# Optimization experiments

Measured on AMD Instinct MI355X. Metric: run time of the kernel, lower is better.

## Reference

```python
import jax, jax.numpy as jnp
import numpy as np

HEADS, HID, OUT_C, IN_C = 8, 128, 2, 64
D = HID // HEADS
NODE = {"cell0": 50000, "cell1": 100000, "cell2": 25000}
# (src_type, dst_type, edge_name, num_edges)
ETYPES = [("cell0", "cell0", "u00", 200000),
          ("cell1", "cell1", "u11", 200000),
          ("cell1", "cell0", "b10", 100000),
          ("cell2", "cell1", "b21", 50000)]


def _segment_softmax(scores, seg, num_segments):
    # numerically-stable softmax over irregular destination segments
    m = jax.ops.segment_max(scores, seg, num_segments=num_segments)
    e = jnp.exp(scores - m[seg])
    s = jax.ops.segment_sum(e, seg, num_segments=num_segments)
    return e / (s[seg] + 1e-16)


def setup_inputs() -> dict:
    key = jax.random.key(0)
    ks = iter(jax.random.split(key, 64))
    s = 0.1
    inp = {}
    for nt, n in NODE.items():
        inp[f"x_{nt}"] = jax.random.normal(next(ks), (n, IN_C), jnp.float32)
    for st, dt, name, e in ETYPES:
        src = jax.random.randint(next(ks), (e,), 0, NODE[st], jnp.int32)
        dst = jax.random.randint(next(ks), (e,), 0, NODE[dt], jnp.int32)
        inp[f"ei_{name}"] = jnp.stack([src, dst])
    # HANConv params: per node-type projection, per edge-type attention vectors
    for nt in NODE:
        inp[f"W_{nt}"] = jax.random.normal(next(ks), (IN_C, HID), jnp.float32) * s
        inp[f"b_{nt}"] = jnp.zeros((HID,), jnp.float32)
    for _, _, name, _ in ETYPES:
        inp[f"as_{name}"] = jax.random.normal(next(ks), (HEADS, D), jnp.float32) * s
        inp[f"ad_{name}"] = jax.random.normal(next(ks), (HEADS, D), jnp.float32) * s
    # semantic attention params + final classifier
    inp["k_w"] = jax.random.normal(next(ks), (HID, HID), jnp.float32) * s
    inp["k_b"] = jnp.zeros((HID,), jnp.float32)
    inp["q"] = jax.random.normal(next(ks), (HID,), jnp.float32) * s
    inp["lin_w"] = jax.random.normal(next(ks), (HID, OUT_C), jnp.float32) * s
    inp["lin_b"] = jnp.zeros((OUT_C,), jnp.float32)
    return inp


def _han_conv(x, ei, W, b, att_s, att_d, k_w, k_b, q):
    # node-level: project each node type -> [N, H, D]
    h = {nt: (x[nt] @ W[nt] + b[nt]).reshape(-1, HEADS, D) for nt in NODE}
    outs = {nt: [] for nt in NODE}
    for st, dt, name, _ in ETYPES:
        xs, xd = h[st], h[dt]
        a_s = (xs * att_s[name]).sum(-1)  # [Ns, H]
        a_d = (xd * att_d[name]).sum(-1)  # [Nd, H]
        src, dst = ei[name][0], ei[name][1]
        alpha = jax.nn.leaky_relu(a_s[src] + a_d[dst], 0.2)  # [E, H]
        alpha = _segment_softmax(alpha, dst, NODE[dt])
        msg = xs[src] * alpha[:, :, None]  # [E, H, D]
        agg = jax.ops.segment_sum(msg, dst, num_segments=NODE[dt])
        outs[dt].append(jax.nn.relu(agg.reshape(-1, HID)))
    # semantic-level attention across metapaths per dst node type
    res = {}
    for nt, lst in outs.items():
        if not lst:
            res[nt] = None
            continue
        stk = jnp.stack(lst)  # [M, N, HID]
        score = (q * jnp.tanh(stk @ k_w + k_b).mean(1)).sum(-1)  # [M]
        attn = jax.nn.softmax(score)
        res[nt] = jnp.einsum('m,mnf->nf', attn, stk)
    return res


def reference(x_cell0, x_cell1, x_cell2,
              W_cell0, b_cell0, W_cell1, b_cell1, W_cell2, b_cell2,
              as_u00, ad_u00, as_u11, ad_u11, as_b10, ad_b10, as_b21, ad_b21,
              k_w, k_b, q, lin_w, lin_b,
              ei_u00, ei_u11, ei_b10, ei_b21):
    x = {"cell0": x_cell0, "cell1": x_cell1, "cell2": x_cell2}
    ei = {"u00": ei_u00, "u11": ei_u11, "b10": ei_b10, "b21": ei_b21}
    W = {"cell0": W_cell0, "cell1": W_cell1, "cell2": W_cell2}
    b = {"cell0": b_cell0, "cell1": b_cell1, "cell2": b_cell2}
    att_s = {"u00": as_u00, "u11": as_u11, "b10": as_b10, "b21": as_b21}
    att_d = {"u00": ad_u00, "u11": ad_u11, "b10": ad_b10, "b21": ad_b21}
    # HAN.forward calls han_conv twice with identical inputs (first result
    # discarded); in eval mode (dropout off) both calls are identical math,
    # so we compute it once.
    out = _han_conv(x, ei, W, b, att_s, att_d, k_w, k_b, q)
    pooled = sum(jnp.sum(v, axis=0) for v in out.values() if v is not None)  # global_add_pool, batch=None
    return jax.nn.sigmoid(pooled[None, :] @ lin_w + lin_b)  # [1, OUT_C]
```

## Files before the change

kernel.cpp:

```cpp
#include <hip/hip_runtime.h>
#include <hip/hip_fp16.h>

#define N0 50000
#define N1 100000
#define N2 25000
#define E00 200000
#define E11 200000
#define E10 100000
#define E21 50000
#define EE  550000
#define ND  300000
#define NB  293
#define NT_ALL 18750
#define HID 128
#define INC 64

typedef _Float16 half8 __attribute__((ext_vector_type(8)));
typedef _Float16 half4_t __attribute__((ext_vector_type(4)));
typedef float float4v __attribute__((ext_vector_type(4)));
typedef float floatx2 __attribute__((ext_vector_type(2)));

struct PrepT {
    const float* W; const float* bias;
    const float* av0; const float* av1; const float* av2; const float* av3;
    _Float16* wtg; _Float16* adtg; float* bdc;
};

__device__ __forceinline__ void decode_edge(
    int e, const int* ei00, const int* ei10, const int* ei11, const int* ei21,
    int& src, int& slot)
{
    if (e < E00)                    { src = ei00[e];               slot = ei00[E00 + e]; }
    else if (e < E00 + E10)         { int i = e - E00;             src = ei10[i]; slot = 50000  + ei10[E10 + i]; }
    else if (e < E00 + E10 + E11)   { int i = e - E00 - E10;       src = ei11[i]; slot = 100000 + ei11[E11 + i]; }
    else                            { int i = e - E00 - E10 - E11; src = ei21[i]; slot = 200000 + ei21[E21 + i]; }
}

__global__ __launch_bounds__(256) void prep_kernel(
    PrepT p0, PrepT p1, PrepT p2,
    const float* __restrict__ kw, const float* __restrict__ lw,
    unsigned char* __restrict__ kwf8,
    const int* __restrict__ ei00, const int* __restrict__ ei10,
    const int* __restrict__ ei11, const int* __restrict__ ei21,
    int* __restrict__ cnt)
{
    if (blockIdx.x >= 32) {
        int e = (blockIdx.x - 32) * 256 + threadIdx.x;
        if (e >= EE) return;
        int src, slot;
        decode_edge(e, ei00, ei10, ei11, ei21, src, slot);
        atomicAdd(&cnt[slot], 1);
        return;
    }
    if (blockIdx.x >= 24) {
        int base = (blockIdx.x - 24) * 256 + threadIdx.x;
        for (int it = 0; it < 9; ++it) {
            int idx = base + it * 2048;
            int f = idx >> 7, g = idx & 127;
            float v;
            if (f < 128)      v = kw[g * 128 + f];
            else if (f < 130) v = lw[g * 2 + (f - 128)];
            else              v = 0.f;
            int r = __builtin_amdgcn_cvt_pk_fp8_f32(v, 0.f, 0, false);
            kwf8[idx] = (unsigned char)r;
        }
        return;
    }
    PrepT P = (blockIdx.x >= 16) ? p2 : (blockIdx.x >= 8) ? p1 : p0;
    const int lb = blockIdx.x & 7;
    const int t2 = lb * 256 + threadIdx.x;
    {
        int f = t2 >> 4, g0 = (t2 & 15) * 4;
        half4_t v;
#pragma unroll
        for (int j = 0; j < 4; ++j) v[j] = (_Float16)P.W[(g0 + j) * 128 + f];
        *(half4_t*)&P.wtg[f * 64 + g0] = v;
    }
    {
        int c = t2 >> 6, g = t2 & 63;
        const float* av = (c < 8) ? P.av0 : (c < 16) ? P.av1 : (c < 24) ? P.av2 : P.av3;
        float v = 0.f;
        if (av) {
            int hh = c & 7;
#pragma unroll
            for (int d = 0; d < 16; ++d)
                v += P.W[g * 128 + hh * 16 + d] * av[hh * 16 + d];
        }
        P.adtg[c * 64 + g] = (_Float16)v;
    }
    if (lb == 0 && threadIdx.x < 32) {
        int c = threadIdx.x;
        const float* av = (c < 8) ? P.av0 : (c < 16) ? P.av1 : (c < 24) ? P.av2 : P.av3;
        float v = 0.f;
        if (av) {
            int hh = c & 7;
#pragma unroll
            for (int d = 0; d < 16; ++d)
                v += P.bias[hh * 16 + d] * av[hh * 16 + d];
        }
        P.bdc[c] = v;
    }
}

struct PT {
    const float* x; const float* bias; unsigned char* h;
    float* ao0; float* ao1; float* ao2; float* ao3;
    const _Float16* wtg; const _Float16* adtg; const float* bdc;
    int N; int ntiles; int bstart; int nblocks;
};

#define HPAD 136
#define PROJ_BLKS 1024

__global__ __launch_bounds__(256, 2) void proj_mfma(
    PT t0, PT t1, PT t2,
    const int* __restrict__ cnt, int* __restrict__ part)
{
    __shared__ _Float16 ht[4][16][HPAD];
    __shared__ int swt[4];
    const int tid = threadIdx.x;
    const int lane = tid & 63, wv = tid >> 6;
    const int fi = lane & 15, hi = lane >> 4;

    if (blockIdx.x >= PROJ_BLKS) {
        const int b = blockIdx.x - PROJ_BLKS;
        int i0 = b * 1024 + tid * 4;
        int s = 0;
#pragma unroll
        for (int k = 0; k < 4; ++k) { int i = i0 + k; s += (i < ND) ? cnt[i] : 0; }
#pragma unroll
        for (int off = 1; off < 64; off <<= 1) s += __shfl_xor(s, off);
        if ((tid & 63) == 0) swt[tid >> 6] = s;
        __syncthreads();
        if (tid == 0) part[b] = swt[0] + swt[1] + swt[2] + swt[3];
        return;
    }

    PT A = (blockIdx.x >= t2.bstart) ? t2 : (blockIdx.x >= t1.bstart) ? t1 : t0;

    half8 bfr[8][2], bd[2][2];
#pragma unroll
    for (int nt = 0; nt < 8; ++nt)
#pragma unroll
        for (int kb = 0; kb < 2; ++kb)
            bfr[nt][kb] = *(const half8*)&A.wtg[(nt * 16 + fi) * 64 + kb * 32 + hi * 8];
#pragma unroll
    for (int t = 0; t < 2; ++t)
#pragma unroll
        for (int kb = 0; kb < 2; ++kb)
            bd[t][kb] = *(const half8*)&A.adtg[(t * 16 + fi) * 64 + kb * 32 + hi * 8];

    float bvv[8];
#pragma unroll
    for (int nt = 0; nt < 8; ++nt) bvv[nt] = A.bias[nt * 16 + fi];
    const float bdc0 = A.bdc[fi];
    const float bdc1 = A.bdc[16 + fi];

    float* aolo = (fi >= 8) ? A.ao1 : A.ao0;
    float* aohi = (fi >= 8) ? A.ao3 : A.ao2;
    const bool has_hi = (A.ao2 != nullptr) || (A.ao3 != nullptr);

    const int stride = A.nblocks * 4;
    for (int t = (blockIdx.x - A.bstart) * 4 + wv; t < A.ntiles; t += stride) {
        const int base = t * 16;
        int rsrc = base + fi; if (rsrc >= A.N) rsrc = A.N - 1;
        const float* xp = A.x + (size_t)rsrc * 64 + hi * 8;
        float4 u0 = *(const float4*)(xp);
        float4 u1 = *(const float4*)(xp + 4);
        float4 u2 = *(const float4*)(xp + 32);
        float4 u3 = *(const float4*)(xp + 36);
        half8 a0, a1;
        a0[0] = (_Float16)u0.x; a0[1] = (_Float16)u0.y; a0[2] = (_Float16)u0.z; a0[3] = (_Float16)u0.w;
        a0[4] = (_Float16)u1.x; a0[5] = (_Float16)u1.y; a0[6] = (_Float16)u1.z; a0[7] = (_Float16)u1.w;
        a1[0] = (_Float16)u2.x; a1[1] = (_Float16)u2.y; a1[2] = (_Float16)u2.z; a1[3] = (_Float16)u2.w;
        a1[4] = (_Float16)u3.x; a1[5] = (_Float16)u3.y; a1[6] = (_Float16)u3.z; a1[7] = (_Float16)u3.w;

        float4v c[8];
#pragma unroll
        for (int nt = 0; nt < 8; ++nt) {
            float4v z = {0.f, 0.f, 0.f, 0.f};
            z = __builtin_amdgcn_mfma_f32_16x16x32_f16(a0, bfr[nt][0], z, 0, 0, 0);
            z = __builtin_amdgcn_mfma_f32_16x16x32_f16(a1, bfr[nt][1], z, 0, 0, 0);
            c[nt] = z;
        }
        float4v d0 = {0.f, 0.f, 0.f, 0.f};
        d0 = __builtin_amdgcn_mfma_f32_16x16x32_f16(a0, bd[0][0], d0, 0, 0, 0);
        d0 = __builtin_amdgcn_mfma_f32_16x16x32_f16(a1, bd[0][1], d0, 0, 0, 0);
        float4v d1 = {0.f, 0.f, 0.f, 0.f};
        if (has_hi) {
            d1 = __builtin_amdgcn_mfma_f32_16x16x32_f16(a0, bd[1][0], d1, 0, 0, 0);
            d1 = __builtin_amdgcn_mfma_f32_16x16x32_f16(a1, bd[1][1], d1, 0, 0, 0);
        }

#pragma unroll
        for (int nt = 0; nt < 8; ++nt)
#pragma unroll
            for (int r = 0; r < 4; ++r)
                ht[wv][hi * 4 + r][nt * 16 + fi] = (_Float16)(c[nt][r] + bvv[nt]);
#pragma unroll
        for (int i = 0; i < 4; ++i) {
            int row = i * 4 + hi;
            int node = base + row;
            if (node < A.N) {
                half8 v = *(const half8*)&ht[wv][row][fi * 8];
                int pa = __builtin_amdgcn_cvt_pk_fp8_f32((float)v[0], (float)v[1], 0, false);
                pa = __builtin_amdgcn_cvt_pk_fp8_f32((float)v[2], (float)v[3], pa, true);
                int pb = __builtin_amdgcn_cvt_pk_fp8_f32((float)v[4], (float)v[5], 0, false);
                pb = __builtin_amdgcn_cvt_pk_fp8_f32((float)v[6], (float)v[7], pb, true);
                int2 o = {pa, pb};
                *(int2*)(A.h + (size_t)node * 128 + fi * 8) = o;
            }
        }
        if (aolo) {
#pragma unroll
            for (int r = 0; r < 4; ++r) {
                int node = base + hi * 4 + r;
                if (node < A.N) aolo[(size_t)node * 8 + (fi & 7)] = d0[r] + bdc0;
            }
        }
        if (aohi) {
#pragma unroll
            for (int r = 0; r < 4; ++r) {
                int node = base + hi * 4 + r;
                if (node < A.N) aohi[(size_t)node * 8 + (fi & 7)] = d1[r] + bdc1;
            }
        }
    }
}

__global__ __launch_bounds__(256) void scan23_kernel(
    const int* __restrict__ cnt, const int* __restrict__ part,
    int* __restrict__ off, int* __restrict__ cursor)
{
    __shared__ int sd[256];
    __shared__ int pex[512];
    __shared__ int wt[4];
    const int tid = threadIdx.x, b = blockIdx.x;
    const int lane = tid & 63, wv = tid >> 6;

    int p0 = (2 * tid     < NB) ? part[2 * tid]     : 0;
    int p1 = (2 * tid + 1 < NB) ? part[2 * tid + 1] : 0;
    int ps = p0 + p1;
    sd[tid] = ps; __syncthreads();
    for (int d = 1; d < 256; d <<= 1) {
        int v = (tid >= d) ? sd[tid - d] : 0;
        __syncthreads();
        sd[tid] += v;
        __syncthreads();
    }
    int exc = sd[tid] - ps;
    pex[2 * tid] = exc;
    pex[2 * tid + 1] = exc + p0;
    __syncthreads();

    int i0 = b * 1024 + tid * 4;
    int v[4];
#pragma unroll
    for (int k = 0; k < 4; ++k) { int i = i0 + k; v[k] = (i < ND) ? cnt[i] : 0; }
    int ts = v[0] + v[1] + v[2] + v[3];
    int inc = ts;
#pragma unroll
    for (int d = 1; d < 64; d <<= 1) {
        int u = __shfl_up(inc, d);
        if (lane >= d) inc += u;
    }
    int wexc = inc - ts;
    if (lane == 63) wt[wv] = inc;
    __syncthreads();
    int wbase = 0;
    for (int w = 0; w < wv; ++w) wbase += wt[w];
    int base = pex[b] + wbase + wexc;
    int pre = 0;
#pragma unroll
    for (int k = 0; k < 4; ++k) {
        int i = i0 + k;
        if (i < ND) { off[i] = base + pre; cursor[i] = base + pre; }
        pre += v[k];
    }
}

__global__ __launch_bounds__(256) void fill_kernel(
    const int* __restrict__ ei00, const int* __restrict__ ei10,
    const int* __restrict__ ei11, const int* __restrict__ ei21,
    const float* __restrict__ as00, const float* __restrict__ ad00,
    const float* __restrict__ as10, const float* __restrict__ ad10,
    const float* __restrict__ as11, const float* __restrict__ ad11,
    const float* __restrict__ as21, const float* __restrict__ ad21,
    int* __restrict__ cursor, int* __restrict__ srcs, _Float16* __restrict__ wgt)
{
    int e = blockIdx.x * 256 + threadIdx.x;
    if (e >= EE) return;
    int src, d, slot;
    const float* asp; const float* adp;
    if (e < E00) {
        src = ei00[e]; d = ei00[E00 + e]; slot = d; asp = as00; adp = ad00;
    } else if (e < E00 + E10) {
        int i = e - E00; src = ei10[i]; d = ei10[E10 + i]; slot = 50000 + d; asp = as10; adp = ad10;
    } else if (e < E00 + E10 + E11) {
        int i = e - E00 - E10; src = ei11[i]; d = ei11[E11 + i]; slot = 100000 + d; asp = as11; adp = ad11;
    } else {
        int i = e - E00 - E10 - E11; src = ei21[i]; d = ei21[E21 + i]; slot = 200000 + d; asp = as21; adp = ad21;
    }
    float4 sa0 = *(const float4*)(asp + (size_t)src * 8);
    float4 sa1 = *(const float4*)(asp + (size_t)src * 8 + 4);
    float4 da0 = *(const float4*)(adp + (size_t)d * 8);
    float4 da1 = *(const float4*)(adp + (size_t)d * 8 + 4);
    float vv[8] = {sa0.x + da0.x, sa0.y + da0.y, sa0.z + da0.z, sa0.w + da0.w,
                   sa1.x + da1.x, sa1.y + da1.y, sa1.z + da1.z, sa1.w + da1.w};
    half8 w;
#pragma unroll
    for (int h = 0; h < 8; ++h) {
        float v = vv[h];
        v = v > 0.f ? v : 0.2f * v;
        w[h] = (_Float16)__expf(v);
    }
    int pos = atomicAdd(&cursor[slot], 1);
    srcs[pos] = src;
    *(half8*)(wgt + (size_t)pos * 8) = w;
}

__global__ __launch_bounds__(256) void gather_kernel(
    const int* __restrict__ cnt, const int* __restrict__ off,
    const int* __restrict__ srcs, const _Float16* __restrict__ wgt,
    const unsigned char* __restrict__ h0, const unsigned char* __restrict__ h1,
    const unsigned char* __restrict__ h2,
    unsigned char* __restrict__ agg)
{
    const int gid = blockIdx.x * 256 + threadIdx.x;
    const int lane = gid & 63;
    const int g8 = lane >> 3, sub = lane & 7;
    const int slot = (gid >> 6) * 8 + g8;
    const unsigned char* hs = (slot < 50000) ? h0 : (slot < 200000) ? h1 : h2;
    const int deg = cnt[slot], st = off[slot];

    int degm = deg;
    degm = max(degm, __shfl_xor(degm, 8));
    degm = max(degm, __shfl_xor(degm, 16));
    degm = max(degm, __shfl_xor(degm, 32));

    float acc[16];
#pragma unroll
    for (int j = 0; j < 16; ++j) acc[j] = 0.f;
    float sw = 0.f;

    int i = 0;
    for (; i + 2 <= degm; i += 2) {
        bool a0 = (i < deg), a1 = (i + 1 < deg);
        int s0 = 0, s1 = 0;
        if (a0) s0 = srcs[st + i];
        if (a1) s1 = srcs[st + i + 1];
        float w0 = 0.f, w1 = 0.f;
        int4 v0 = {0, 0, 0, 0}, v1 = {0, 0, 0, 0};
        if (a0) { w0 = (float)wgt[(size_t)(st + i) * 8 + sub];
                  v0 = *(const int4*)(hs + (size_t)s0 * 128 + sub * 16); }
        if (a1) { w1 = (float)wgt[(size_t)(st + i + 1) * 8 + sub];
                  v1 = *(const int4*)(hs + (size_t)s1 * 128 + sub * 16); }
        const int wa[4] = {v0.x, v0.y, v0.z, v0.w};
        const int wb[4] = {v1.x, v1.y, v1.z, v1.w};
#pragma unroll
        for (int k = 0; k < 4; ++k) {
            floatx2 fa0 = __builtin_amdgcn_cvt_pk_f32_fp8(wa[k], false);
            floatx2 fa1 = __builtin_amdgcn_cvt_pk_f32_fp8(wa[k], true);
            floatx2 fb0 = __builtin_amdgcn_cvt_pk_f32_fp8(wb[k], false);
            floatx2 fb1 = __builtin_amdgcn_cvt_pk_f32_fp8(wb[k], true);
            acc[4 * k + 0] += w0 * fa0.x + w1 * fb0.x;
            acc[4 * k + 1] += w0 * fa0.y + w1 * fb0.y;
            acc[4 * k + 2] += w0 * fa1.x + w1 * fb1.x;
            acc[4 * k + 3] += w0 * fa1.y + w1 * fb1.y;
        }
        sw += w0 + w1;
    }
    if (i < degm) {
        bool a0 = (i < deg);
        int s0 = 0;
        if (a0) s0 = srcs[st + i];
        float w0 = 0.f;
        int4 v0 = {0, 0, 0, 0};
        if (a0) { w0 = (float)wgt[(size_t)(st + i) * 8 + sub];
                  v0 = *(const int4*)(hs + (size_t)s0 * 128 + sub * 16); }
        const int wa[4] = {v0.x, v0.y, v0.z, v0.w};
#pragma unroll
        for (int k = 0; k < 4; ++k) {
            floatx2 fa0 = __builtin_amdgcn_cvt_pk_f32_fp8(wa[k], false);
            floatx2 fa1 = __builtin_amdgcn_cvt_pk_f32_fp8(wa[k], true);
            acc[4 * k + 0] += w0 * fa0.x;
            acc[4 * k + 1] += w0 * fa0.y;
            acc[4 * k + 2] += w0 * fa1.x;
            acc[4 * k + 3] += w0 * fa1.y;
        }
        sw += w0;
    }

    float rr = __builtin_amdgcn_rcpf(sw + 1e-16f);
    int4 o;
    int pk[4];
#pragma unroll
    for (int k = 0; k < 4; ++k) {
        float r0 = fmaxf(acc[4 * k + 0] * rr, 0.f);
        float r1 = fmaxf(acc[4 * k + 1] * rr, 0.f);
        float r2 = fmaxf(acc[4 * k + 2] * rr, 0.f);
        float r3 = fmaxf(acc[4 * k + 3] * rr, 0.f);
        int p = __builtin_amdgcn_cvt_pk_fp8_f32(r0, r1, 0, false);
        p = __builtin_amdgcn_cvt_pk_fp8_f32(r2, r3, p, true);
        pk[k] = p;
    }
    o.x = pk[0]; o.y = pk[1]; o.z = pk[2]; o.w = pk[3];
    *(int4*)(agg + (size_t)slot * 128 + sub * 16) = o;
}

#define ASTR 144
__global__ __launch_bounds__(256, 2) void semantic_kernel(
    const unsigned char* __restrict__ agg, const unsigned char* __restrict__ kwf8,
    const float* __restrict__ kb, const float* __restrict__ q,
    const float* __restrict__ lb,
    float* __restrict__ cs2, float* __restrict__ score,
    unsigned int* __restrict__ done, float* __restrict__ out)
{
    __shared__ char abuf[2][16 * ASTR];
    __shared__ float redv[12];
    const int tid = threadIdx.x;
    const int lane = tid & 63, wv = tid >> 6;
    const int fi = lane & 15, hi = lane >> 4;

    if (tid < 12) redv[tid] = 0.f;

    const int ftbase = wv * 2;
    const int nft = (wv == 3) ? 3 : 2;

    long bf[3][4];
    float qv[3], kbv[3];
#pragma unroll
    for (int i = 0; i < 3; ++i) {
        if (i < nft) {
            int ft = ftbase + i;
#pragma unroll
            for (int kk = 0; kk < 4; ++kk)
                bf[i][kk] = *(const long*)&kwf8[(ft * 16 + fi) * 128 + kk * 32 + hi * 8];
            qv[i]  = (ft < 8) ? q[ft * 16 + fi]  : 0.f;
            kbv[i] = (ft < 8) ? kb[ft * 16 + fi] : 0.f;
        } else {
            bf[i][0] = bf[i][1] = bf[i][2] = bf[i][3] = 0;
            qv[i] = 0.f; kbv[i] = 0.f;
        }
    }

    float sc[4] = {0.f, 0.f, 0.f, 0.f};
    float cs[4] = {0.f, 0.f, 0.f, 0.f};

    const int s_off = (tid >> 4) * ASTR + (tid & 15) * 8;
    const int a_off = fi * ASTR + hi * 8;

    int t = blockIdx.x;
    const int stride = gridDim.x;
    if (t < NT_ALL) {
        long areg = *(const long*)(agg + (size_t)t * 2048 + tid * 8);
        *(long*)&abuf[0][s_off] = areg;
    }
    __syncthreads();
    int cur = 0;
    while (t < NT_ALL) {
        const int tn = t + stride;
        long aregn = 0;
        if (tn < NT_ALL)
            aregn = *(const long*)(agg + (size_t)tn * 2048 + tid * 8);

        long af[4];
#pragma unroll
        for (int kk = 0; kk < 4; ++kk)
            af[kk] = *(const long*)&abuf[cur][a_off + kk * 32];

        const int m = (t >= 12500) ? 3 : (t >= 6250) ? 2 : (t >= 3125) ? 1 : 0;
        float tsc = 0.f, tcs = 0.f;
#pragma unroll
        for (int i = 0; i < 3; ++i) {
            if (i >= nft) continue;
            float4v c = {0.f, 0.f, 0.f, 0.f};
            c = __builtin_amdgcn_mfma_f32_16x16x32_fp8_fp8(af[0], bf[i][0], c, 0, 0, 0);
            c = __builtin_amdgcn_mfma_f32_16x16x32_fp8_fp8(af[1], bf[i][1], c, 0, 0, 0);
            c = __builtin_amdgcn_mfma_f32_16x16x32_fp8_fp8(af[2], bf[i][2], c, 0, 0, 0);
            c = __builtin_amdgcn_mfma_f32_16x16x32_fp8_fp8(af[3], bf[i][3], c, 0, 0, 0);
            if (ftbase + i == 8) {
                tcs = c[0] + c[1] + c[2] + c[3];
            } else {
#pragma unroll
                for (int r = 0; r < 4; ++r) {
                    float y = c[r] + kbv[i];
                    float e = __expf(2.f * y);
                    tsc += qv[i] * (1.f - 2.f * __builtin_amdgcn_rcpf(e + 1.f));
                }
            }
        }
        if (m == 0)      { sc[0] += tsc; cs[0] += tcs; }
        else if (m == 1) { sc[1] += tsc; cs[1] += tcs; }
        else if (m == 2) { sc[2] += tsc; cs[2] += tcs; }
        else             { sc[3] += tsc; cs[3] += tcs; }

        if (tn < NT_ALL)
            *(long*)&abuf[cur ^ 1][s_off] = aregn;
        __syncthreads();
        cur ^= 1;
        t = tn;
    }

#pragma unroll
    for (int m = 0; m < 4; ++m) {
        float s = sc[m];
#pragma unroll
        for (int off = 1; off < 64; off <<= 1) s += __shfl_xor(s, off);
        if (lane == 0 && s != 0.f) atomicAdd(&redv[m], s);
        float v = cs[m];
        v += __shfl_xor(v, 16);
        v += __shfl_xor(v, 32);
        if (hi == 0 && fi < 2 && v != 0.f) atomicAdd(&redv[4 + 2 * m + fi], v);
    }
    __syncthreads();
    if (tid < 4)              atomicAdd(&score[tid], redv[tid]);
    if (tid >= 4 && tid < 12) atomicAdd(&cs2[tid - 4], redv[tid]);

    __syncthreads();
    if (tid == 0) {
        __threadfence();
        unsigned int old = atomicAdd(done, 1u);
        if (old == gridDim.x - 1) {
            __threadfence();
            float s0 = score[0] / (float)N0;
            float s1 = score[1] / (float)N0;
            float s2 = score[2] / (float)N1;
            float s3 = score[3] / (float)N1;
            float m0 = fmaxf(s0, s1);
            float e0 = __expf(s0 - m0), e1 = __expf(s1 - m0);
            float a0 = e0 / (e0 + e1), a1 = e1 / (e0 + e1);
            float m1 = fmaxf(s2, s3);
            float e2 = __expf(s2 - m1), e3 = __expf(s3 - m1);
            float a2 = e2 / (e2 + e3), a3 = e3 / (e2 + e3);
            float z0 = a0 * cs2[0] + a1 * cs2[2] + a2 * cs2[4] + a3 * cs2[6] + lb[0];
            float z1 = a0 * cs2[1] + a1 * cs2[3] + a2 * cs2[5] + a3 * cs2[7] + lb[1];
            out[0] = 1.f / (1.f + __expf(-z0));
            out[1] = 1.f / (1.f + __expf(-z1));
        }
    }
}

extern "C" void kernel_launch(void* const* d_in, const int* in_sizes, int n_in,
                              void* d_out, int out_size, void* d_ws, size_t ws_size,
                              hipStream_t stream)
{
    const float* x0  = (const float*)d_in[0];
    const float* x1  = (const float*)d_in[1];
    const float* x2  = (const float*)d_in[2];
    const int* ei00  = (const int*)d_in[3];
    const int* ei11  = (const int*)d_in[4];
    const int* ei10  = (const int*)d_in[5];
    const int* ei21  = (const int*)d_in[6];
    const float* W0  = (const float*)d_in[7];  const float* b0 = (const float*)d_in[8];
    const float* W1  = (const float*)d_in[9];  const float* b1 = (const float*)d_in[10];
    const float* W2  = (const float*)d_in[11]; const float* b2 = (const float*)d_in[12];
    const float* as00 = (const float*)d_in[13]; const float* ad00 = (const float*)d_in[14];
    const float* as11 = (const float*)d_in[15]; const float* ad11 = (const float*)d_in[16];
    const float* as10 = (const float*)d_in[17]; const float* ad10 = (const float*)d_in[18];
    const float* as21 = (const float*)d_in[19]; const float* ad21 = (const float*)d_in[20];
    const float* kw  = (const float*)d_in[21]; const float* kb  = (const float*)d_in[22];
    const float* q   = (const float*)d_in[23];
    const float* lw  = (const float*)d_in[24]; const float* lb  = (const float*)d_in[25];
    float* out = (float*)d_out;

    char* p = (char*)d_ws;
    auto alloc = [&](size_t bytes) {
        char* r = p;
        p += (bytes + 255) & ~(size_t)255;
        return r;
    };
    unsigned char* h0 = (unsigned char*)alloc((size_t)N0 * 128);
    unsigned char* h1 = (unsigned char*)alloc((size_t)N1 * 128);
    unsigned char* h2 = (unsigned char*)alloc((size_t)N2 * 128);
    float* o_as00 = (float*)alloc((size_t)N0 * 32);
    float* o_ad00 = (float*)alloc((size_t)N0 * 32);
    float* o_as11 = (float*)alloc((size_t)N1 * 32);
    float* o_ad11 = (float*)alloc((size_t)N1 * 32);
    float* o_as10 = (float*)alloc((size_t)N1 * 32);
    float* o_ad10 = (float*)alloc((size_t)N0 * 32);
    float* o_as21 = (float*)alloc((size_t)N2 * 32);
    float* o_ad21 = (float*)alloc((size_t)N1 * 32);
    int* off    = (int*)alloc((size_t)ND * 4);
    int* cursor = (int*)alloc((size_t)ND * 4);
    int* part   = (int*)alloc((size_t)512 * 4);
    int* srcs   = (int*)alloc((size_t)EE * 4);
    _Float16* wgt = (_Float16*)alloc((size_t)EE * 16);
    unsigned char* agg = (unsigned char*)alloc((size_t)ND * 128);
    _Float16* wtg0 = (_Float16*)alloc(128 * 64 * 2);
    _Float16* wtg1 = (_Float16*)alloc(128 * 64 * 2);
    _Float16* wtg2 = (_Float16*)alloc(128 * 64 * 2);
    _Float16* adtg0 = (_Float16*)alloc(32 * 64 * 2);
    _Float16* adtg1 = (_Float16*)alloc(32 * 64 * 2);
    _Float16* adtg2 = (_Float16*)alloc(32 * 64 * 2);
    float* bdcg = (float*)alloc(3 * 32 * 4);
    unsigned char* kwf8 = (unsigned char*)alloc(144 * 128);
    char* zstart = p;
    int* cnt = (int*)alloc((size_t)ND * 4);
    float* colsum2 = (float*)alloc(8 * 4);
    float* score   = (float*)alloc(4 * 4);
    unsigned int* done = (unsigned int*)alloc(4);
    size_t zbytes = (size_t)(p - zstart);

    (void)hipMemsetAsync(zstart, 0, zbytes, stream);

    PrepT pp0 = {W0, b0, as00, ad00, ad10, nullptr, wtg0, adtg0, bdcg + 0};
    PrepT pp1 = {W1, b1, as11, ad11, as10, ad21,    wtg1, adtg1, bdcg + 32};
    PrepT pp2 = {W2, b2, as21, nullptr, nullptr, nullptr, wtg2, adtg2, bdcg + 64};
    prep_kernel<<<32 + (EE + 255) / 256, 256, 0, stream>>>(
        pp0, pp1, pp2, kw, lw, kwf8, ei00, ei10, ei11, ei21, cnt);

    PT t0 = {x0, b0, h0,
             o_as00, o_ad00, o_ad10, nullptr,
             wtg0, adtg0, bdcg + 0,
             N0, 3125, 0, 296};
    PT t1 = {x1, b1, h1,
             o_as11, o_ad11, o_as10, o_ad21,
             wtg1, adtg1, bdcg + 32,
             N1, 6250, 296, 584};
    PT t2 = {x2, b2, h2,
             o_as21, nullptr, nullptr, nullptr,
             wtg2, adtg2, bdcg + 64,
             N2, 1563, 880, 144};
    proj_mfma<<<PROJ_BLKS + NB, 256, 0, stream>>>(t0, t1, t2, cnt, part);

    scan23_kernel<<<NB, 256, 0, stream>>>(cnt, part, off, cursor);

    fill_kernel<<<(EE + 255) / 256, 256, 0, stream>>>(ei00, ei10, ei11, ei21,
        o_as00, o_ad00, o_as10, o_ad10, o_as11, o_ad11, o_as21, o_ad21,
        cursor, srcs, wgt);

    gather_kernel<<<ND / 32, 256, 0, stream>>>(cnt, off, srcs, wgt, h0, h1, h2, agg);

    semantic_kernel<<<2048, 256, 0, stream>>>(agg, kwf8, kb, q, lb,
                                              colsum2, score, done, out);
}
```

Measured before the change: 301.9 us.

## Fuse gather aggregation with semantic attention scoring via shared-memory tile

Merges the gather kernel and the semantic kernel into one launch. Each block aggregates 32 destination slots, writes the fp8 results into an LDS tile, and runs the semantic MFMA scoring on that tile in place. This removes the global round-trip of the aggregated buffer and one kernel launch. In exchange every one of the 9375 blocks reloads the kw weights from global or cache, pays extra block-level and global atomic reductions, and increments the done counter, where the old semantic kernel used 2048 persistent blocks.

New measurement: 458.8 us. 52.0% more time.

```diff
diff --git a/kernel.cpp b/kernel.cpp
--- a/kernel.cpp
+++ b/kernel.cpp
@@ -11,7 +11,6 @@
 #define EE  550000
 #define ND  300000
 #define NB  293
-#define NT_ALL 18750
 #define HID 128
 #define INC 64
 
@@ -319,17 +318,27 @@
     *(half8*)(wgt + (size_t)pos * 8) = w;
 }
 
-__global__ __launch_bounds__(256) void gather_kernel(
+#define ATSTR 136
+__global__ __launch_bounds__(256) void gather_sem_kernel(
     const int* __restrict__ cnt, const int* __restrict__ off,
     const int* __restrict__ srcs, const _Float16* __restrict__ wgt,
     const unsigned char* __restrict__ h0, const unsigned char* __restrict__ h1,
     const unsigned char* __restrict__ h2,
-    unsigned char* __restrict__ agg)
-{
-    const int gid = blockIdx.x * 256 + threadIdx.x;
-    const int lane = gid & 63;
+    const unsigned char* __restrict__ kwf8,
+    const float* __restrict__ kb, const float* __restrict__ q,
+    const float* __restrict__ lb,
+    float* __restrict__ cs2, float* __restrict__ score,
+    unsigned int* __restrict__ done, float* __restrict__ out)
+{
+    __shared__ char atile[32 * ATSTR];
+    __shared__ float redv[12];
+    const int tid = threadIdx.x;
+    const int lane = tid & 63, wv = tid >> 6;
+
+    if (tid < 12) redv[tid] = 0.f;
+
     const int g8 = lane >> 3, sub = lane & 7;
-    const int slot = (gid >> 6) * 8 + g8;
+    const int slot = blockIdx.x * 32 + wv * 8 + g8;
     const unsigned char* hs = (slot < 50000) ? h0 : (slot < 200000) ? h1 : h2;
     const int deg = cnt[slot], st = off[slot];
 
@@ -392,7 +401,6 @@
     }
 
     float rr = __builtin_amdgcn_rcpf(sw + 1e-16f);
-    int4 o;
     int pk[4];
 #pragma unroll
     for (int k = 0; k < 4; ++k) {
@@ -404,118 +412,59 @@
         p = __builtin_amdgcn_cvt_pk_fp8_f32(r2, r3, p, true);
         pk[k] = p;
     }
-    o.x = pk[0]; o.y = pk[1]; o.z = pk[2]; o.w = pk[3];
-    *(int4*)(agg + (size_t)slot * 128 + sub * 16) = o;
-}
-
-#define ASTR 144
-__global__ __launch_bounds__(256, 2) void semantic_kernel(
-    const unsigned char* __restrict__ agg, const unsigned char* __restrict__ kwf8,
-    const float* __restrict__ kb, const float* __restrict__ q,
-    const float* __restrict__ lb,
-    float* __restrict__ cs2, float* __restrict__ score,
-    unsigned int* __restrict__ done, float* __restrict__ out)
-{
-    __shared__ char abuf[2][16 * ASTR];
-    __shared__ float redv[12];
-    const int tid = threadIdx.x;
-    const int lane = tid & 63, wv = tid >> 6;
+    {
+        int4 o; o.x = pk[0]; o.y = pk[1]; o.z = pk[2]; o.w = pk[3];
+        *(int4*)&atile[(wv * 8 + g8) * ATSTR + sub * 16] = o;
+    }
+    __syncthreads();
+
     const int fi = lane & 15, hi = lane >> 4;
-
-    if (tid < 12) redv[tid] = 0.f;
-
-    const int ftbase = wv * 2;
-    const int nft = (wv == 3) ? 3 : 2;
-
-    long bf[3][4];
-    float qv[3], kbv[3];
-#pragma unroll
-    for (int i = 0; i < 3; ++i) {
-        if (i < nft) {
-            int ft = ftbase + i;
-#pragma unroll
-            for (int kk = 0; kk < 4; ++kk)
-                bf[i][kk] = *(const long*)&kwf8[(ft * 16 + fi) * 128 + kk * 32 + hi * 8];
-            qv[i]  = (ft < 8) ? q[ft * 16 + fi]  : 0.f;
-            kbv[i] = (ft < 8) ? kb[ft * 16 + fi] : 0.f;
+    const int tw = wv >> 1;
+    const int t = blockIdx.x * 2 + tw;
+    const int m = (t >= 12500) ? 3 : (t >= 6250) ? 2 : (t >= 3125) ? 1 : 0;
+
+    long af[4];
+#pragma unroll
+    for (int kk = 0; kk < 4; ++kk)
+        af[kk] = *(const long*)&atile[(tw * 16 + fi) * ATSTR + hi * 8 + kk * 32];
+
+    const int ftb = (wv & 1) ? 5 : 0;
+    const int nft = (wv & 1) ? 4 : 5;
+    float tsc = 0.f, tcs = 0.f;
+    for (int ii = 0; ii < nft; ++ii) {
+        const int ft = ftb + ii;
+        long b0 = *(const long*)&kwf8[(ft * 16 + fi) * 128 + 0 * 32 + hi * 8];
+        long b1 = *(const long*)&kwf8[(ft * 16 + fi) * 128 + 1 * 32 + hi * 8];
+        long b2 = *(const long*)&kwf8[(ft * 16 + fi) * 128 + 2 * 32 + hi * 8];
+        long b3 = *(const long*)&kwf8[(ft * 16 + fi) * 128 + 3 * 32 + hi * 8];
+        float4v c = {0.f, 0.f, 0.f, 0.f};
+        c = __builtin_amdgcn_mfma_f32_16x16x32_fp8_fp8(af[0], b0, c, 0, 0, 0);
+        c = __builtin_amdgcn_mfma_f32_16x16x32_fp8_fp8(af[1], b1, c, 0, 0, 0);
+        c = __builtin_amdgcn_mfma_f32_16x16x32_fp8_fp8(af[2], b2, c, 0, 0, 0);
+        c = __builtin_amdgcn_mfma_f32_16x16x32_fp8_fp8(af[3], b3, c, 0, 0, 0);
+        if (ft == 8) {
+            tcs = c[0] + c[1] + c[2] + c[3];
         } else {
-            bf[i][0] = bf[i][1] = bf[i][2] = bf[i][3] = 0;
-            qv[i] = 0.f; kbv[i] = 0.f;
-        }
-    }
-
-    float sc[4] = {0.f, 0.f, 0.f, 0.f};
-    float cs[4] = {0.f, 0.f, 0.f, 0.f};
-
-    const int s_off = (tid >> 4) * ASTR + (tid & 15) * 8;
-    const int a_off = fi * ASTR + hi * 8;
-
-    int t = blockIdx.x;
-    const int stride = gridDim.x;
-    if (t < NT_ALL) {
-        long areg = *(const long*)(agg + (size_t)t * 2048 + tid * 8);
-        *(long*)&abuf[0][s_off] = areg;
-    }
+            float qv = q[ft * 16 + fi];
+            float kbv = kb[ft * 16 + fi];
+#pragma unroll
+            for (int r = 0; r < 4; ++r) {
+                float y = c[r] + kbv;
+                float e = __expf(2.f * y);
+                tsc += qv * (1.f - 2.f * __builtin_amdgcn_rcpf(e + 1.f));
+            }
+        }
+    }
+
+#pragma unroll
+    for (int o = 1; o < 64; o <<= 1) tsc += __shfl_xor(tsc, o);
+    if (lane == 0 && tsc != 0.f) atomicAdd(&redv[m], tsc);
+    tcs += __shfl_xor(tcs, 16);
+    tcs += __shfl_xor(tcs, 32);
+    if ((wv & 1) && hi == 0 && fi < 2 && tcs != 0.f) atomicAdd(&redv[4 + 2 * m + fi], tcs);
     __syncthreads();
-    int cur = 0;
-    while (t < NT_ALL) {
-        const int tn = t + stride;
-        long aregn = 0;
-        if (tn < NT_ALL)
-            aregn = *(const long*)(agg + (size_t)tn * 2048 + tid * 8);
-
-        long af[4];
-#pragma unroll
-        for (int kk = 0; kk < 4; ++kk)
-            af[kk] = *(const long*)&abuf[cur][a_off + kk * 32];
-
-        const int m = (t >= 12500) ? 3 : (t >= 6250) ? 2 : (t >= 3125) ? 1 : 0;
-        float tsc = 0.f, tcs = 0.f;
-#pragma unroll
-        for (int i = 0; i < 3; ++i) {
-            if (i >= nft) continue;
-            float4v c = {0.f, 0.f, 0.f, 0.f};
-            c = __builtin_amdgcn_mfma_f32_16x16x32_fp8_fp8(af[0], bf[i][0], c, 0, 0, 0);
-            c = __builtin_amdgcn_mfma_f32_16x16x32_fp8_fp8(af[1], bf[i][1], c, 0, 0, 0);
-            c = __builtin_amdgcn_mfma_f32_16x16x32_fp8_fp8(af[2], bf[i][2], c, 0, 0, 0);
-            c = __builtin_amdgcn_mfma_f32_16x16x32_fp8_fp8(af[3], bf[i][3], c, 0, 0, 0);
-            if (ftbase + i == 8) {
-                tcs = c[0] + c[1] + c[2] + c[3];
-            } else {
-#pragma unroll
-                for (int r = 0; r < 4; ++r) {
-                    float y = c[r] + kbv[i];
-                    float e = __expf(2.f * y);
-                    tsc += qv[i] * (1.f - 2.f * __builtin_amdgcn_rcpf(e + 1.f));
-                }
-            }
-        }
-        if (m == 0)      { sc[0] += tsc; cs[0] += tcs; }
-        else if (m == 1) { sc[1] += tsc; cs[1] += tcs; }
-        else if (m == 2) { sc[2] += tsc; cs[2] += tcs; }
-        else             { sc[3] += tsc; cs[3] += tcs; }
-
-        if (tn < NT_ALL)
-            *(long*)&abuf[cur ^ 1][s_off] = aregn;
-        __syncthreads();
-        cur ^= 1;
-        t = tn;
-    }
-
-#pragma unroll
-    for (int m = 0; m < 4; ++m) {
-        float s = sc[m];
-#pragma unroll
-        for (int off = 1; off < 64; off <<= 1) s += __shfl_xor(s, off);
-        if (lane == 0 && s != 0.f) atomicAdd(&redv[m], s);
-        float v = cs[m];
-        v += __shfl_xor(v, 16);
-        v += __shfl_xor(v, 32);
-        if (hi == 0 && fi < 2 && v != 0.f) atomicAdd(&redv[4 + 2 * m + fi], v);
-    }
-    __syncthreads();
-    if (tid < 4)              atomicAdd(&score[tid], redv[tid]);
-    if (tid >= 4 && tid < 12) atomicAdd(&cs2[tid - 4], redv[tid]);
+    if (tid < 4 && redv[tid] != 0.f)               atomicAdd(&score[tid], redv[tid]);
+    if (tid >= 4 && tid < 12 && redv[tid] != 0.f)  atomicAdd(&cs2[tid - 4], redv[tid]);
 
     __syncthreads();
     if (tid == 0) {
@@ -586,7 +535,6 @@
     int* part   = (int*)alloc((size_t)512 * 4);
     int* srcs   = (int*)alloc((size_t)EE * 4);
     _Float16* wgt = (_Float16*)alloc((size_t)EE * 16);
-    unsigned char* agg = (unsigned char*)alloc((size_t)ND * 128);
     _Float16* wtg0 = (_Float16*)alloc(128 * 64 * 2);
     _Float16* wtg1 = (_Float16*)alloc(128 * 64 * 2);
     _Float16* wtg2 = (_Float16*)alloc(128 * 64 * 2);
@@ -630,8 +578,6 @@
         o_as00, o_ad00, o_as10, o_ad10, o_as11, o_ad11, o_as21, o_ad21,
         cursor, srcs, wgt);
 
-    gather_kernel<<<ND / 32, 256, 0, stream>>>(cnt, off, srcs, wgt, h0, h1, h2, agg);
-
-    semantic_kernel<<<2048, 256, 0, stream>>>(agg, kwf8, kb, q, lb,
-                                              colsum2, score, done, out);
-}
+    gather_sem_kernel<<<ND / 32, 256, 0, stream>>>(cnt, off, srcs, wgt,
+        h0, h1, h2, kwf8, kb, q, lb, colsum2, score, done, out);
+}
```
